# Kernel tuning notes

Measured on AMD Instinct MI355X. Metric: run time of the kernel, lower is better.

## Reference

```python
import jax, jax.numpy as jnp
import numpy as np

ATTENTION_HEAD = 16
EXPANSION_LENGTH = 300
TEXT_EMBEDDING_DIM = 768
LN_EPS = 1e-3  # keras LayerNormalization default epsilon


def setup_inputs() -> dict:
    key = jax.random.key(0)
    ks = jax.random.split(key, 8)
    B, L, D = 8, 2048, TEXT_EMBEDDING_DIM
    H = ATTENTION_HEAD
    E = EXPANSION_LENGTH
    dh = D // H
    glorot = lambda k, shape, fan_in, fan_out: jax.random.uniform(
        k, shape, jnp.float32,
        -jnp.sqrt(6.0 / (fan_in + fan_out)), jnp.sqrt(6.0 / (fan_in + fan_out)))
    return {
        "q": jax.random.normal(ks[0], (B, 1, L, D), jnp.float32),
        "k": jax.random.normal(ks[1], (B, 1, L, D), jnp.float32),
        "v": jax.random.normal(ks[2], (B, 1, L, D), jnp.float32),
        "Wq": glorot(ks[3], (D, D), D, D),
        "bq": jnp.zeros((D,), jnp.float32),
        "Wv": glorot(ks[4], (D, D), D, D),
        "bv": jnp.zeros((D,), jnp.float32),
        "memory": glorot(ks[5], (E, H, dh), E, dh),
        "gamma": jnp.ones((D,), jnp.float32),
        "beta": jnp.zeros((D,), jnp.float32),
    }


def reference(q, k, v, Wq, bq, Wv, bv, memory, gamma, beta):
    B, _, L, D = q.shape
    H = ATTENTION_HEAD
    dh = D // H
    # Dense projections (v is unused by the original module)
    Q_ = q @ Wq + bq                      # (B,1,L,D)
    V_ = k @ Wv + bv                      # (B,1,L,D)
    Q = Q_.reshape(B, L, H, dh)
    V = V_.reshape(B, L, H, dh)
    # memory-query scores, ReLU instead of softmax
    eij = jax.nn.relu(jnp.einsum('ehd,blhd->belh', memory, Q))  # (B,E,L,H)
    out1 = jnp.einsum('belh,blhd->behd', eij, V)                # (B,E,H,dh)
    out2 = jnp.einsum('behd,belh->blhd', out1, eij)             # (B,L,H,dh)
    x = out2.reshape(B, 1, L, D)
    mean = jnp.mean(x, axis=-1, keepdims=True)
    var = jnp.var(x, axis=-1, keepdims=True)
    return (x - mean) * jax.lax.rsqrt(var + LN_EPS) * gamma + beta
```

## Files before the change

kernel.cpp:

```cpp
#include <hip/hip_runtime.h>
#include <hip/hip_bf16.h>
#include <stdint.h>

#define B_   8
#define L_   2048
#define D_   768
#define H_   16
#define DH   48
#define E_   300
#define EP   320
#define KP   64
#define ACH  4
#define N1T  (128 * DH * EP)
#define NT_  24

typedef __bf16 bf16;
typedef __bf16 bf16x8 __attribute__((ext_vector_type(8)));
typedef __bf16 bf16x4 __attribute__((ext_vector_type(4)));
typedef float  f32x4  __attribute__((ext_vector_type(4)));

typedef const __attribute__((address_space(1))) uint32_t guint;
typedef __attribute__((address_space(3))) uint32_t luint;

__device__ __forceinline__ f32x4 mfma16(bf16x8 a, bf16x8 b, f32x4 c) {
  return __builtin_amdgcn_mfma_f32_16x16x32_bf16(a, b, c, 0, 0, 0);
}

__global__ __launch_bounds__(256) void k_wt(const float* __restrict__ Wq,
                                            const float* __restrict__ Wv,
                                            bf16* __restrict__ WqT,
                                            bf16* __restrict__ WvT) {
  int idx = blockIdx.x * 256 + threadIdx.x;
  int n = idx / D_, k = idx % D_;
  const float* W = blockIdx.y ? Wv : Wq;
  bf16* WT = blockIdx.y ? WvT : WqT;
  WT[n * D_ + k] = (bf16)W[k * D_ + n];
}

__global__ __launch_bounds__(256) void k_mem(const float* __restrict__ M,
                                             bf16* __restrict__ MP) {
  int idx = blockIdx.x * 256 + threadIdx.x;
  int h = idx / (EP * KP);
  int r = idx % (EP * KP);
  int e = r / KP, d = r % KP;
  float v = (e < E_ && d < DH) ? M[(e * H_ + h) * DH + d] : 0.f;
  MP[idx] = (bf16)v;
}

__global__ __launch_bounds__(512, 2) void k_gemm(
    const float* __restrict__ A0, const float* __restrict__ A1,
    const bf16* __restrict__ WT0, const bf16* __restrict__ WT1,
    const float* __restrict__ b0, const float* __restrict__ b1,
    bf16* __restrict__ outQ, bf16* __restrict__ outVT) {
  __shared__ float Asf[3][128 * 32];
  __shared__ bf16  Bs[3][256 * 32];
  const int tid = threadIdx.x, lane = tid & 63, w = tid >> 6;
  const int wr = w >> 2, wc = w & 3;
  const int lr = lane & 15, lq = lane >> 4;
  const int bid = blockIdx.x;
  const int j = (bid & 7) * 48 + (bid >> 3);
  const int n0 = (j % 3) * 256, m0 = (j / 3) * 128;
  const int mode = blockIdx.y;
  const float* A = mode ? A1 : A0;
  const bf16* WT = mode ? WT1 : WT0;
  const float* bias = mode ? b1 : b0;

  auto stage = [&](int buf, int k0) {
#pragma unroll
    for (int t = 0; t < 2; ++t) {
      int idx = tid + t * 512;
      int row = idx >> 3, s4 = idx & 7;
      int g4 = s4 ^ ((row >> 1) & 7);
      const float* src = A + (size_t)(m0 + row) * D_ + k0 + g4 * 4;
      __builtin_amdgcn_global_load_lds((guint*)src,
          (luint*)&Asf[buf][(t * 512 + w * 64) * 4], 16, 0, 0);
    }
#pragma unroll
    for (int t = 0; t < 2; ++t) {
      int idx = tid + t * 512;
      int row = idx >> 2, s8 = idx & 3;
      int g8 = s8 ^ ((row >> 1) & 3);
      const bf16* src = WT + (size_t)(n0 + row) * D_ + k0 + g8 * 8;
      __builtin_amdgcn_global_load_lds((guint*)src,
          (luint*)&Bs[buf][(t * 512 + w * 64) * 8], 16, 0, 0);
    }
  };

  f32x4 acc[4][4] = {};

  stage(0, 0);
  stage(1, 32);

  for (int t = 0; t < NT_; ++t) {
    const int cur = t % 3;
    if (t + 1 < NT_)
      asm volatile("s_waitcnt vmcnt(4) lgkmcnt(0)" ::: "memory");
    else
      asm volatile("s_waitcnt vmcnt(0) lgkmcnt(0)" ::: "memory");
    __builtin_amdgcn_s_barrier();
    __builtin_amdgcn_sched_barrier(0);
    if (t + 2 < NT_) stage((t + 2) % 3, (t + 2) * 32);

    bf16x8 af[4], bfr[4];
#pragma unroll
    for (int mi = 0; mi < 4; ++mi) {
      int row = wr * 64 + mi * 16 + lr;
      int sw = (row >> 1) & 7;
      float4 p0 = *(const float4*)&Asf[cur][row * 32 + (((lq * 2) ^ sw) * 4)];
      float4 p1 = *(const float4*)&Asf[cur][row * 32 + (((lq * 2 + 1) ^ sw) * 4)];
      bf16x8 v;
      v[0] = (bf16)p0.x; v[1] = (bf16)p0.y; v[2] = (bf16)p0.z; v[3] = (bf16)p0.w;
      v[4] = (bf16)p1.x; v[5] = (bf16)p1.y; v[6] = (bf16)p1.z; v[7] = (bf16)p1.w;
      af[mi] = v;
    }
#pragma unroll
    for (int ni = 0; ni < 4; ++ni) {
      int row = wc * 64 + ni * 16 + lr;
      bfr[ni] = *(const bf16x8*)&Bs[cur][row * 32 + ((lq ^ ((row >> 1) & 3)) * 8)];
    }
#pragma unroll
    for (int mi = 0; mi < 4; ++mi)
#pragma unroll
      for (int ni = 0; ni < 4; ++ni)
        acc[mi][ni] = mfma16(af[mi], bfr[ni], acc[mi][ni]);
  }

  float bs[4];
#pragma unroll
  for (int ni = 0; ni < 4; ++ni) bs[ni] = bias[n0 + wc * 64 + ni * 16 + lr];

  if (mode == 0) {
#pragma unroll
    for (int mi = 0; mi < 4; ++mi)
#pragma unroll
      for (int ni = 0; ni < 4; ++ni) {
        int m = m0 + wr * 64 + mi * 16 + lq * 4;
        int n = n0 + wc * 64 + ni * 16 + lr;
#pragma unroll
        for (int r = 0; r < 4; ++r)
          outQ[(size_t)(m + r) * D_ + n] = (bf16)(acc[mi][ni][r] + bs[ni]);
      }
  } else {
#pragma unroll
    for (int mi = 0; mi < 4; ++mi)
#pragma unroll
      for (int ni = 0; ni < 4; ++ni) {
        int mb = m0 + wr * 64 + mi * 16 + lq * 4;
        int n = n0 + wc * 64 + ni * 16 + lr;
        int bhd = (mb >> 11) * H_ + n / DH;
        int d = n % DH;
        int l = mb & (L_ - 1);
        bf16x4 v;
#pragma unroll
        for (int r = 0; r < 4; ++r) v[r] = (bf16)(acc[mi][ni][r] + bs[ni]);
        *(bf16x4*)&outVT[((size_t)bhd * DH + d) * L_ + l] = v;
      }
  }
}

__global__ __launch_bounds__(256) void k_phaseA(
    const bf16* __restrict__ Qb, const bf16* __restrict__ VT,
    const bf16* __restrict__ MP, float* __restrict__ O1P) {
  __shared__ bf16 Qs[2][32 * 88];
  __shared__ bf16 Vs[2][48 * 40];
  __shared__ bf16 Ss[EP * 40];
  const int tid = threadIdx.x, lane = tid & 63, w = tid >> 6;
  const int lr = lane & 15, lq = lane >> 4;
  const int bh = blockIdx.y, b = bh >> 4, h = bh & 15;
  const int lbase = blockIdx.x * (L_ / ACH);

  bf16x8 mf[5][2];
#pragma unroll
  for (int mi = 0; mi < 5; ++mi)
#pragma unroll
    for (int kh = 0; kh < 2; ++kh)
      mf[mi][kh] = *(const bf16x8*)&MP[(size_t)(h * EP + w * 80 + mi * 16 + lr) * KP + kh * 32 + lq * 8];

  if (tid < 128) {
    int buf = tid >> 6, t = tid & 63;
    uint4 z = {0, 0, 0, 0};
    *(uint4*)&Qs[buf][(t >> 1) * 88 + 48 + (t & 1) * 8] = z;
  }

  auto loadQ = [&](int idx, int l0) {
    return *(const bf16x8*)&Qb[(size_t)(b * L_ + l0 + idx / 6) * D_ + h * DH + (idx % 6) * 8];
  };
  auto loadV = [&](int j, int l0) {
    return *(const bf16x8*)&VT[((size_t)bh * DH + (j >> 2)) * L_ + l0 + (j & 3) * 8];
  };

  bf16x8 rA, rB;
  {
    int l0 = lbase;
    rA = (tid < 192) ? loadQ(tid, l0) : loadV(tid - 192, l0);
    if (tid < 128) rB = loadV(tid + 64, l0);
  }

  f32x4 acc[5][3] = {};

  for (int it = 0; it < L_ / ACH / 32; ++it) {
    const int cur = it & 1;
    if (tid < 192) *(bf16x8*)&Qs[cur][(tid / 6) * 88 + (tid % 6) * 8] = rA;
    else           *(bf16x8*)&Vs[cur][((tid - 192) >> 2) * 40 + ((tid - 192) & 3) * 8] = rA;
    if (tid < 128) *(bf16x8*)&Vs[cur][((tid + 64) >> 2) * 40 + ((tid + 64) & 3) * 8] = rB;
    __syncthreads();
    if (it + 1 < L_ / ACH / 32) {
      int l0 = lbase + (it + 1) * 32;
      rA = (tid < 192) ? loadQ(tid, l0) : loadV(tid - 192, l0);
      if (tid < 128) rB = loadV(tid + 64, l0);
    }
    bf16x8 qf[2][2];
#pragma unroll
    for (int ni = 0; ni < 2; ++ni)
#pragma unroll
      for (int kh = 0; kh < 2; ++kh)
        qf[ni][kh] = *(const bf16x8*)&Qs[cur][(ni * 16 + lr) * 88 + kh * 32 + lq * 8];
#pragma unroll
    for (int mi = 0; mi < 5; ++mi)
#pragma unroll
      for (int ni = 0; ni < 2; ++ni) {
        f32x4 s = {0.f, 0.f, 0.f, 0.f};
        s = mfma16(mf[mi][0], qf[ni][0], s);
        s = mfma16(mf[mi][1], qf[ni][1], s);
#pragma unroll
        for (int r = 0; r < 4; ++r)
          Ss[(w * 80 + mi * 16 + lq * 4 + r) * 40 + ni * 16 + lr] =
              (bf16)(s[r] > 0.f ? s[r] : 0.f);
      }
    bf16x8 sf[5], vf[3];
#pragma unroll
    for (int mi = 0; mi < 5; ++mi)
      sf[mi] = *(const bf16x8*)&Ss[(w * 80 + mi * 16 + lr) * 40 + lq * 8];
#pragma unroll
    for (int ni = 0; ni < 3; ++ni)
      vf[ni] = *(const bf16x8*)&Vs[cur][(ni * 16 + lr) * 40 + lq * 8];
#pragma unroll
    for (int mi = 0; mi < 5; ++mi)
#pragma unroll
      for (int ni = 0; ni < 3; ++ni)
        acc[mi][ni] = mfma16(sf[mi], vf[ni], acc[mi][ni]);
  }
  float* dst = O1P + (size_t)(blockIdx.x * 128 + bh) * DH * EP;
#pragma unroll
  for (int mi = 0; mi < 5; ++mi)
#pragma unroll
    for (int ni = 0; ni < 3; ++ni) {
      int e = w * 80 + mi * 16 + lq * 4;
      int d = ni * 16 + lr;
#pragma unroll
      for (int r = 0; r < 4; ++r)
        dst[(size_t)d * EP + e + r] = acc[mi][ni][r];
    }
}

__global__ __launch_bounds__(256) void k_red(const float* __restrict__ O1P,
                                             bf16* __restrict__ O1T) {
  int idx = blockIdx.x * 256 + threadIdx.x;
  if (idx >= N1T) return;
  float s = O1P[idx];
#pragma unroll
  for (int c = 1; c < ACH; ++c) s += O1P[(size_t)c * N1T + idx];
  O1T[idx] = (bf16)s;
}

__global__ __launch_bounds__(256, 4) void k_phaseB(
    const bf16* __restrict__ Qb, const bf16* __restrict__ MP,
    const bf16* __restrict__ O1T, bf16* __restrict__ X) {
  __shared__ bf16 Qs[64 * 88];
  __shared__ bf16 STs[64 * 76];
  __shared__ bf16 O1s[2][48 * 76];
  const int tid = threadIdx.x, lane = tid & 63, w = tid >> 6;
  const int lr = lane & 15, lq = lane >> 4;
  const int bh = blockIdx.y, b = bh >> 4, h = bh & 15;
  const int l0 = blockIdx.x * 64;

  bf16x8 mfB[5][2];
#pragma unroll
  for (int c = 0; c < 5; ++c)
#pragma unroll
    for (int kh = 0; kh < 2; ++kh)
      mfB[c][kh] = *(const bf16x8*)&MP[(size_t)(h * EP + c * 64 + w * 16 + lr) * KP + kh * 32 + lq * 8];

  for (int idx = tid; idx < 512; idx += 256) {
    if (idx < 384) {
      int row = idx / 6, c = idx % 6;
      *(bf16x8*)&Qs[row * 88 + c * 8] =
          *(const bf16x8*)&Qb[(size_t)(b * L_ + l0 + row) * D_ + h * DH + c * 8];
    } else {
      int j = idx - 384;
      uint4 z = {0, 0, 0, 0};
      *(uint4*)&Qs[(j >> 1) * 88 + 48 + (j & 1) * 8] = z;
    }
  }
  for (int idx = tid; idx < 384; idx += 256)
    *(bf16x8*)&O1s[0][(idx >> 3) * 76 + (idx & 7) * 8] =
        *(const bf16x8*)&O1T[((size_t)bh * DH + (idx >> 3)) * EP + (idx & 7) * 8];
  __syncthreads();

  f32x4 acc[3] = {};
#pragma unroll
  for (int c = 0; c < 5; ++c) {
    bf16x8 r0, r1;
    if (c < 4) {
      r0 = *(const bf16x8*)&O1T[((size_t)bh * DH + (tid >> 3)) * EP + (c + 1) * 64 + (tid & 7) * 8];
      if (tid < 128) {
        int i2 = tid + 256;
        r1 = *(const bf16x8*)&O1T[((size_t)bh * DH + (i2 >> 3)) * EP + (c + 1) * 64 + (i2 & 7) * 8];
      }
    }
#pragma unroll
    for (int mi = 0; mi < 4; ++mi) {
      bf16x8 qa0 = *(const bf16x8*)&Qs[(mi * 16 + lr) * 88 + lq * 8];
      bf16x8 qa1 = *(const bf16x8*)&Qs[(mi * 16 + lr) * 88 + 32 + lq * 8];
      f32x4 s = {0.f, 0.f, 0.f, 0.f};
      s = mfma16(qa0, mfB[c][0], s);
      s = mfma16(qa1, mfB[c][1], s);
#pragma unroll
      for (int r = 0; r < 4; ++r)
        STs[(mi * 16 + lq * 4 + r) * 76 + w * 16 + lr] =
            (bf16)(s[r] > 0.f ? s[r] : 0.f);
    }
    __syncthreads();
#pragma unroll
    for (int ks = 0; ks < 2; ++ks) {
      bf16x8 sf = *(const bf16x8*)&STs[(w * 16 + lr) * 76 + ks * 32 + lq * 8];
#pragma unroll
      for (int ni = 0; ni < 3; ++ni) {
        bf16x8 of = *(const bf16x8*)&O1s[c & 1][(ni * 16 + lr) * 76 + ks * 32 + lq * 8];
        acc[ni] = mfma16(sf, of, acc[ni]);
      }
    }
    if (c < 4) {
      *(bf16x8*)&O1s[(c + 1) & 1][(tid >> 3) * 76 + (tid & 7) * 8] = r0;
      if (tid < 128) {
        int i2 = tid + 256;
        *(bf16x8*)&O1s[(c + 1) & 1][(i2 >> 3) * 76 + (i2 & 7) * 8] = r1;
      }
    }
    __syncthreads();
  }
#pragma unroll
  for (int ni = 0; ni < 3; ++ni)
#pragma unroll
    for (int r = 0; r < 4; ++r)
      X[(size_t)(b * L_ + l0 + w * 16 + lq * 4 + r) * D_ + h * DH + ni * 16 + lr] =
          (bf16)acc[ni][r];
}

__global__ __launch_bounds__(256) void k_ln(
    const bf16* __restrict__ X, const float* __restrict__ gamma,
    const float* __restrict__ beta, float* __restrict__ out) {
  const int lane = threadIdx.x & 63;
  const int row = blockIdx.x * 4 + (threadIdx.x >> 6);
  const bf16* x = X + (size_t)row * D_;
  float v[12];
#pragma unroll
  for (int c = 0; c < 3; ++c) {
    bf16x4 ch = *(const bf16x4*)(x + lane * 12 + c * 4);
#pragma unroll
    for (int j = 0; j < 4; ++j) v[c * 4 + j] = (float)ch[j];
  }
  float s = 0.f, q = 0.f;
#pragma unroll
  for (int j = 0; j < 12; ++j) { s += v[j]; q += v[j] * v[j]; }
#pragma unroll
  for (int off = 32; off > 0; off >>= 1) {
    s += __shfl_xor(s, off);
    q += __shfl_xor(q, off);
  }
  float mean = s * (1.f / 768.f);
  float var = q * (1.f / 768.f) - mean * mean;
  float inv = rsqrtf(var + 1e-3f);
  float* o = out + (size_t)row * D_;
#pragma unroll
  for (int c = 0; c < 3; ++c) {
    float4 g = *(const float4*)(gamma + lane * 12 + c * 4);
    float4 bt = *(const float4*)(beta + lane * 12 + c * 4);
    float4 r;
    r.x = (v[c * 4 + 0] - mean) * inv * g.x + bt.x;
    r.y = (v[c * 4 + 1] - mean) * inv * g.y + bt.y;
    r.z = (v[c * 4 + 2] - mean) * inv * g.z + bt.z;
    r.w = (v[c * 4 + 3] - mean) * inv * g.w + bt.w;
    *(float4*)(o + lane * 12 + c * 4) = r;
  }
}

extern "C" void kernel_launch(void* const* d_in, const int* in_sizes, int n_in,
                              void* d_out, int out_size, void* d_ws, size_t ws_size,
                              hipStream_t stream) {
  (void)in_sizes; (void)n_in; (void)out_size; (void)ws_size;
  const float* q_in = (const float*)d_in[0];
  const float* k_in = (const float*)d_in[1];
  const float* Wq   = (const float*)d_in[3];
  const float* bq   = (const float*)d_in[4];
  const float* Wv   = (const float*)d_in[5];
  const float* bv   = (const float*)d_in[6];
  const float* mem  = (const float*)d_in[7];
  const float* gam  = (const float*)d_in[8];
  const float* bet  = (const float*)d_in[9];
  float* out = (float*)d_out;

  char* ws = (char*)d_ws;
  size_t off = 0;
  auto alloc = [&](size_t bytes) {
    char* p = ws + off;
    off += (bytes + 255) & ~(size_t)255;
    return p;
  };
  bf16*  WqT = (bf16*)alloc((size_t)D_ * D_ * 2);
  bf16*  WvT = (bf16*)alloc((size_t)D_ * D_ * 2);
  bf16*  MP  = (bf16*)alloc((size_t)H_ * EP * KP * 2);
  bf16*  Qb  = (bf16*)alloc((size_t)B_ * L_ * D_ * 2);
  bf16*  VT  = (bf16*)alloc((size_t)B_ * H_ * DH * L_ * 2);
  bf16*  O1T = (bf16*)alloc((size_t)N1T * 2);
  const size_t o1pBytes = (size_t)ACH * N1T * 4;
  const size_t xbBytes  = (size_t)B_ * L_ * D_ * 2;
  char*  big = alloc(xbBytes > o1pBytes ? xbBytes : o1pBytes);
  float* O1P = (float*)big;
  bf16*  Xb  = (bf16*)big;

  k_wt<<<dim3((D_ * D_) / 256, 2), 256, 0, stream>>>(Wq, Wv, WqT, WvT);
  k_mem<<<(H_ * EP * KP) / 256, 256, 0, stream>>>(mem, MP);
  k_gemm<<<dim3(384, 2), 512, 0, stream>>>(q_in, k_in, WqT, WvT, bq, bv, Qb, VT);
  k_phaseA<<<dim3(ACH, B_ * H_), 256, 0, stream>>>(Qb, VT, MP, O1P);
  k_red<<<(N1T + 255) / 256, 256, 0, stream>>>(O1P, O1T);
  k_phaseB<<<dim3(L_ / 64, B_ * H_), 256, 0, stream>>>(Qb, MP, O1T, Xb);
  k_ln<<<(B_ * L_) / 4, 256, 0, stream>>>(Xb, gam, bet, out);
}
```

Baseline: 205.2 us.

## Pre-cast activations to bf16, retile GEMM, bf16 phase-A partials with more splits

Adds a standalone kernel that casts q and k to bf16 up front, so the projection GEMM loads bf16 A tiles directly instead of converting fp32 in LDS. The GEMM is retiled to 128x128 tiles on 256-thread blocks with more blocks per CU. Phase A now uses 8 L-chunks instead of 4 and writes its partials as bf16, and the reduction kernel is vectorised to match. The extra cast pass adds a full read and write of both inputs. The bf16 partials lose some accuracy in the reduction.

```diff
diff --git a/kernel.cpp b/kernel.cpp
--- a/kernel.cpp
+++ b/kernel.cpp
@@ -10,7 +10,7 @@
 #define E_   300
 #define EP   320
 #define KP   64
-#define ACH  4
+#define ACH  8
 #define N1T  (128 * DH * EP)
 #define NT_  24
 
@@ -24,6 +24,23 @@
 
 __device__ __forceinline__ f32x4 mfma16(bf16x8 a, bf16x8 b, f32x4 c) {
   return __builtin_amdgcn_mfma_f32_16x16x32_bf16(a, b, c, 0, 0, 0);
+}
+
+__global__ __launch_bounds__(256) void k_cast(const float* __restrict__ q,
+                                              const float* __restrict__ k,
+                                              bf16* __restrict__ qc,
+                                              bf16* __restrict__ kc) {
+  const float* src = blockIdx.y ? k : q;
+  bf16* dst = blockIdx.y ? kc : qc;
+  const int n8 = B_ * L_ * D_ / 8;
+  for (int i = blockIdx.x * 256 + threadIdx.x; i < n8; i += gridDim.x * 256) {
+    float4 f0 = *(const float4*)(src + (size_t)i * 8);
+    float4 f1 = *(const float4*)(src + (size_t)i * 8 + 4);
+    bf16x8 v;
+    v[0] = (bf16)f0.x; v[1] = (bf16)f0.y; v[2] = (bf16)f0.z; v[3] = (bf16)f0.w;
+    v[4] = (bf16)f1.x; v[5] = (bf16)f1.y; v[6] = (bf16)f1.z; v[7] = (bf16)f1.w;
+    *(bf16x8*)(dst + (size_t)i * 8) = v;
+  }
 }
 
 __global__ __launch_bounds__(256) void k_wt(const float* __restrict__ Wq,
@@ -47,42 +64,42 @@
   MP[idx] = (bf16)v;
 }
 
-__global__ __launch_bounds__(512, 2) void k_gemm(
-    const float* __restrict__ A0, const float* __restrict__ A1,
+__global__ __launch_bounds__(256, 3) void k_gemm(
+    const bf16* __restrict__ A0, const bf16* __restrict__ A1,
     const bf16* __restrict__ WT0, const bf16* __restrict__ WT1,
     const float* __restrict__ b0, const float* __restrict__ b1,
     bf16* __restrict__ outQ, bf16* __restrict__ outVT) {
-  __shared__ float Asf[3][128 * 32];
-  __shared__ bf16  Bs[3][256 * 32];
+  __shared__ bf16 As[3][128 * 32];
+  __shared__ bf16 Bs[3][128 * 32];
   const int tid = threadIdx.x, lane = tid & 63, w = tid >> 6;
-  const int wr = w >> 2, wc = w & 3;
+  const int wr = w >> 1, wc = w & 1;
   const int lr = lane & 15, lq = lane >> 4;
   const int bid = blockIdx.x;
-  const int j = (bid & 7) * 48 + (bid >> 3);
-  const int n0 = (j % 3) * 256, m0 = (j / 3) * 128;
+  const int j = (bid & 7) * 96 + (bid >> 3);
+  const int n0 = (j % 6) * 128, m0 = (j / 6) * 128;
   const int mode = blockIdx.y;
-  const float* A = mode ? A1 : A0;
+  const bf16* A = mode ? A1 : A0;
   const bf16* WT = mode ? WT1 : WT0;
   const float* bias = mode ? b1 : b0;
 
   auto stage = [&](int buf, int k0) {
 #pragma unroll
-    for (int t = 0; t < 2; ++t) {
-      int idx = tid + t * 512;
-      int row = idx >> 3, s4 = idx & 7;
-      int g4 = s4 ^ ((row >> 1) & 7);
-      const float* src = A + (size_t)(m0 + row) * D_ + k0 + g4 * 4;
+    for (int p = 0; p < 2; ++p) {
+      int idx = tid + p * 256;
+      int row = idx >> 2, ct = idx & 3;
+      int gc = ct ^ ((row >> 1) & 3);
+      const bf16* src = A + (size_t)(m0 + row) * D_ + k0 + gc * 8;
       __builtin_amdgcn_global_load_lds((guint*)src,
-          (luint*)&Asf[buf][(t * 512 + w * 64) * 4], 16, 0, 0);
-    }
-#pragma unroll
-    for (int t = 0; t < 2; ++t) {
-      int idx = tid + t * 512;
-      int row = idx >> 2, s8 = idx & 3;
-      int g8 = s8 ^ ((row >> 1) & 3);
-      const bf16* src = WT + (size_t)(n0 + row) * D_ + k0 + g8 * 8;
+          (luint*)&As[buf][(p * 256 + w * 64) * 8], 16, 0, 0);
+    }
+#pragma unroll
+    for (int p = 0; p < 2; ++p) {
+      int idx = tid + p * 256;
+      int row = idx >> 2, ct = idx & 3;
+      int gc = ct ^ ((row >> 1) & 3);
+      const bf16* src = WT + (size_t)(n0 + row) * D_ + k0 + gc * 8;
       __builtin_amdgcn_global_load_lds((guint*)src,
-          (luint*)&Bs[buf][(t * 512 + w * 64) * 8], 16, 0, 0);
+          (luint*)&Bs[buf][(p * 256 + w * 64) * 8], 16, 0, 0);
     }
   };
 
@@ -93,10 +110,8 @@
 
   for (int t = 0; t < NT_; ++t) {
     const int cur = t % 3;
-    if (t + 1 < NT_)
-      asm volatile("s_waitcnt vmcnt(4) lgkmcnt(0)" ::: "memory");
-    else
-      asm volatile("s_waitcnt vmcnt(0) lgkmcnt(0)" ::: "memory");
+    if (t + 1 < NT_) asm volatile("s_waitcnt vmcnt(4) lgkmcnt(0)" ::: "memory");
+    else             asm volatile("s_waitcnt vmcnt(0) lgkmcnt(0)" ::: "memory");
     __builtin_amdgcn_s_barrier();
     __builtin_amdgcn_sched_barrier(0);
     if (t + 2 < NT_) stage((t + 2) % 3, (t + 2) * 32);
@@ -105,13 +120,7 @@
 #pragma unroll
     for (int mi = 0; mi < 4; ++mi) {
       int row = wr * 64 + mi * 16 + lr;
-      int sw = (row >> 1) & 7;
-      float4 p0 = *(const float4*)&Asf[cur][row * 32 + (((lq * 2) ^ sw) * 4)];
-      float4 p1 = *(const float4*)&Asf[cur][row * 32 + (((lq * 2 + 1) ^ sw) * 4)];
-      bf16x8 v;
-      v[0] = (bf16)p0.x; v[1] = (bf16)p0.y; v[2] = (bf16)p0.z; v[3] = (bf16)p0.w;
-      v[4] = (bf16)p1.x; v[5] = (bf16)p1.y; v[6] = (bf16)p1.z; v[7] = (bf16)p1.w;
-      af[mi] = v;
+      af[mi] = *(const bf16x8*)&As[cur][row * 32 + ((lq ^ ((row >> 1) & 3)) * 8)];
     }
 #pragma unroll
     for (int ni = 0; ni < 4; ++ni) {
@@ -160,7 +169,7 @@
 
 __global__ __launch_bounds__(256) void k_phaseA(
     const bf16* __restrict__ Qb, const bf16* __restrict__ VT,
-    const bf16* __restrict__ MP, float* __restrict__ O1P) {
+    const bf16* __restrict__ MP, bf16* __restrict__ O1P) {
   __shared__ bf16 Qs[2][32 * 88];
   __shared__ bf16 Vs[2][48 * 40];
   __shared__ bf16 Ss[EP * 40];
@@ -240,27 +249,35 @@
       for (int ni = 0; ni < 3; ++ni)
         acc[mi][ni] = mfma16(sf[mi], vf[ni], acc[mi][ni]);
   }
-  float* dst = O1P + (size_t)(blockIdx.x * 128 + bh) * DH * EP;
+  bf16* dst = O1P + (size_t)(blockIdx.x * 128 + bh) * DH * EP;
 #pragma unroll
   for (int mi = 0; mi < 5; ++mi)
 #pragma unroll
     for (int ni = 0; ni < 3; ++ni) {
       int e = w * 80 + mi * 16 + lq * 4;
       int d = ni * 16 + lr;
-#pragma unroll
-      for (int r = 0; r < 4; ++r)
-        dst[(size_t)d * EP + e + r] = acc[mi][ni][r];
-    }
-}
-
-__global__ __launch_bounds__(256) void k_red(const float* __restrict__ O1P,
+      bf16x4 v;
+#pragma unroll
+      for (int r = 0; r < 4; ++r) v[r] = (bf16)acc[mi][ni][r];
+      *(bf16x4*)&dst[(size_t)d * EP + e] = v;
+    }
+}
+
+__global__ __launch_bounds__(256) void k_red(const bf16* __restrict__ O1P,
                                              bf16* __restrict__ O1T) {
-  int idx = blockIdx.x * 256 + threadIdx.x;
-  if (idx >= N1T) return;
-  float s = O1P[idx];
-#pragma unroll
-  for (int c = 1; c < ACH; ++c) s += O1P[(size_t)c * N1T + idx];
-  O1T[idx] = (bf16)s;
+  int i8 = blockIdx.x * 256 + threadIdx.x;
+  if (i8 >= N1T / 8) return;
+  float s[8] = {};
+#pragma unroll
+  for (int c = 0; c < ACH; ++c) {
+    bf16x8 v = *(const bf16x8*)&O1P[(size_t)c * N1T + (size_t)i8 * 8];
+#pragma unroll
+    for (int j = 0; j < 8; ++j) s[j] += (float)v[j];
+  }
+  bf16x8 o;
+#pragma unroll
+  for (int j = 0; j < 8; ++j) o[j] = (bf16)s[j];
+  *(bf16x8*)&O1T[(size_t)i8 * 8] = o;
 }
 
 __global__ __launch_bounds__(256, 4) void k_phaseB(
@@ -413,17 +430,22 @@
   bf16*  Qb  = (bf16*)alloc((size_t)B_ * L_ * D_ * 2);
   bf16*  VT  = (bf16*)alloc((size_t)B_ * H_ * DH * L_ * 2);
   bf16*  O1T = (bf16*)alloc((size_t)N1T * 2);
-  const size_t o1pBytes = (size_t)ACH * N1T * 4;
-  const size_t xbBytes  = (size_t)B_ * L_ * D_ * 2;
-  char*  big = alloc(xbBytes > o1pBytes ? xbBytes : o1pBytes);
-  float* O1P = (float*)big;
+  const size_t castHalf  = ((size_t)B_ * L_ * D_ * 2 + 256) & ~(size_t)255;
+  const size_t castBytes = 2 * castHalf;
+  const size_t o1pBytes  = (size_t)ACH * N1T * 2;
+  size_t bigBytes = castBytes > o1pBytes ? castBytes : o1pBytes;
+  char*  big = alloc(bigBytes);
+  bf16*  qc  = (bf16*)big;
+  bf16*  kc  = (bf16*)(big + castHalf);
+  bf16*  O1P = (bf16*)big;
   bf16*  Xb  = (bf16*)big;
 
+  k_cast<<<dim3(2048, 2), 256, 0, stream>>>(q_in, k_in, qc, kc);
   k_wt<<<dim3((D_ * D_) / 256, 2), 256, 0, stream>>>(Wq, Wv, WqT, WvT);
   k_mem<<<(H_ * EP * KP) / 256, 256, 0, stream>>>(mem, MP);
-  k_gemm<<<dim3(384, 2), 512, 0, stream>>>(q_in, k_in, WqT, WvT, bq, bv, Qb, VT);
+  k_gemm<<<dim3(768, 2), 256, 0, stream>>>(qc, kc, WqT, WvT, bq, bv, Qb, VT);
   k_phaseA<<<dim3(ACH, B_ * H_), 256, 0, stream>>>(Qb, VT, MP, O1P);
-  k_red<<<(N1T + 255) / 256, 256, 0, stream>>>(O1P, O1T);
+  k_red<<<(N1T / 8 + 255) / 256, 256, 0, stream>>>(O1P, O1T);
   k_phaseB<<<dim3(L_ / 64, B_ * H_), 256, 0, stream>>>(Qb, MP, O1T, Xb);
   k_ln<<<(B_ * L_) / 4, 256, 0, stream>>>(Xb, gam, bet, out);
 }
```

Result: faster. 190.7 us (-7.1%).
